# Kernel tuning notes

Measured on AMD Instinct MI355X. Metric: run time of the kernel, lower is better.

Reference implementation:

```python
import jax, jax.numpy as jnp
import numpy as np

N_NODES = 100000
N_EDGES = 1600000
IN_DIM, HIDDEN, OUT_DIM = 128, 64, 32


def setup_inputs() -> dict:
    key = jax.random.key(0)
    k1, k2, k3, k4 = jax.random.split(key, 4)
    x = jax.random.normal(k1, (N_NODES, IN_DIM), dtype=jnp.float32)
    # Glorot-style init for the two GCN linear layers
    W1 = jax.random.normal(k2, (IN_DIM, HIDDEN), dtype=jnp.float32) * (1.0 / np.sqrt(IN_DIM))
    b1 = jnp.zeros((HIDDEN,), dtype=jnp.float32)
    W2 = jax.random.normal(k3, (HIDDEN, OUT_DIM), dtype=jnp.float32) * (1.0 / np.sqrt(HIDDEN))
    b2 = jnp.zeros((OUT_DIM,), dtype=jnp.float32)
    edge_index = jax.random.randint(k4, (2, N_EDGES), 0, N_NODES, dtype=jnp.int32)
    return {"x": x, "W1": W1, "b1": b1, "W2": W2, "b2": b2, "edge_index": edge_index}


def _gcn_norm(edge_index, n_nodes):
    # Add self-loops and compute symmetric normalization D^{-1/2} (A+I) D^{-1/2}
    loops = jnp.arange(n_nodes, dtype=edge_index.dtype)
    src = jnp.concatenate([edge_index[0], loops])  # [E+N]
    dst = jnp.concatenate([edge_index[1], loops])
    deg = jax.ops.segment_sum(jnp.ones_like(dst, dtype=jnp.float32), dst,
                              num_segments=n_nodes)
    dinv = jnp.where(deg > 0, jax.lax.rsqrt(deg), 0.0)
    norm = dinv[src] * dinv[dst]  # [E+N]
    return src, dst, norm


def _gcn_conv(h, W, b, src, dst, norm, n_nodes):
    h = h @ W                                   # [N, out] linear transform first
    msg = h[src] * norm[:, None]                # gather + per-edge scale
    agg = jax.ops.segment_sum(msg, dst, num_segments=n_nodes)  # scatter-add
    return agg + b


def reference(x, W1, b1, W2, b2, edge_index):
    n = x.shape[0]
    src, dst, norm = _gcn_norm(edge_index, n)
    h = jax.nn.relu(_gcn_conv(x, W1, b1, src, dst, norm, n))
    # dropout is identity in eval mode (deterministic reference)
    z = _gcn_conv(h, W2, b2, src, dst, norm, n)
    return z
```

## Files before the change

kernel.cpp:

```cpp
#include <hip/hip_runtime.h>
#include <hip/hip_fp16.h>

#define NB_MAX 784
#define CAP    2560
#define CHUNK  8192

typedef _Float16 half8 __attribute__((ext_vector_type(8)));
typedef float f32x4_t __attribute__((ext_vector_type(4)));
typedef int   i32x4   __attribute__((ext_vector_type(4)));

__device__ inline int   ntld (const int*   p) { return __builtin_nontemporal_load(p); }
__device__ inline i32x4 ntld4(const int*   p) { return __builtin_nontemporal_load((const i32x4*)p); }

__global__ __launch_bounds__(256) void k_bin_gemm1(
        const int* __restrict__ src, const int* __restrict__ dst,
        int* __restrict__ gcur, int* __restrict__ binned, int nb, int e,
        const float* __restrict__ x, const float* __restrict__ W1,
        __half* __restrict__ hp, int n, int binb) {
    __shared__ __align__(16) char smem[64 * 136 * 2];
    const int t = threadIdx.x;

    if (blockIdx.x < binb) {
        int* hist = (int*)smem;
        int* curs = hist + NB_MAX;
        const int base = blockIdx.x * CHUNK;
        const int lim = min(CHUNK, e - base);

        for (int i = t; i < NB_MAX; i += 256) hist[i] = 0;
        __syncthreads();

        const int i4lim = lim >> 2;
        for (int i = t; i < i4lim; i += 256) {
            int4 d = ((const int4*)(dst + base))[i];
            atomicAdd(&hist[d.x >> 7], 1);
            atomicAdd(&hist[d.y >> 7], 1);
            atomicAdd(&hist[d.z >> 7], 1);
            atomicAdd(&hist[d.w >> 7], 1);
        }
        for (int i = (i4lim << 2) + t; i < lim; i += 256)
            atomicAdd(&hist[dst[base + i] >> 7], 1);
        __syncthreads();

        for (int b = t; b < nb; b += 256) {
            int h = hist[b];
            curs[b] = h ? atomicAdd(&gcur[b], h) : 0;
        }
        __syncthreads();

        for (int i = t; i < i4lim; i += 256) {
            i32x4 d = ntld4(dst + base + i * 4);
            i32x4 s = ntld4(src + base + i * 4);
            int o0 = atomicAdd(&curs[d.x >> 7], 1);
            int o1 = atomicAdd(&curs[d.y >> 7], 1);
            int o2 = atomicAdd(&curs[d.z >> 7], 1);
            int o3 = atomicAdd(&curs[d.w >> 7], 1);
            if (o0 < CAP) binned[(size_t)(d.x >> 7) * CAP + o0] = (s.x << 7) | (d.x & 127);
            if (o1 < CAP) binned[(size_t)(d.y >> 7) * CAP + o1] = (s.y << 7) | (d.y & 127);
            if (o2 < CAP) binned[(size_t)(d.z >> 7) * CAP + o2] = (s.z << 7) | (d.z & 127);
            if (o3 < CAP) binned[(size_t)(d.w >> 7) * CAP + o3] = (s.w << 7) | (d.w & 127);
        }
        for (int i = (i4lim << 2) + t; i < lim; i += 256) {
            int d = dst[base + i], s = src[base + i];
            int off = atomicAdd(&curs[d >> 7], 1);
            if (off < CAP) binned[(size_t)(d >> 7) * CAP + off] = (s << 7) | (d & 127);
        }
        return;
    }

    _Float16* wt = (_Float16*)smem;

    for (int i = t; i < 128 * 64; i += 256) {
        int k = i >> 6, o = i & 63;
        wt[o * 136 + k] = (_Float16)W1[i];
    }
    __syncthreads();

    const int lane = t & 63;
    const int wid  = t >> 6;
    const int row0 = (blockIdx.x - binb) * 64 + wid * 16;
    const int rA   = lane & 15;
    const int g    = lane >> 4;

    f32x4_t acc0 = {0.f, 0.f, 0.f, 0.f};
    f32x4_t acc1 = {0.f, 0.f, 0.f, 0.f};
    f32x4_t acc2 = {0.f, 0.f, 0.f, 0.f};
    f32x4_t acc3 = {0.f, 0.f, 0.f, 0.f};

    const int arow = min(row0 + rA, n - 1);
    const float* ap0 = x + (size_t)arow * 128 + g * 8;

#pragma unroll
    for (int ks = 0; ks < 4; ++ks) {
        const float* ap = ap0 + ks * 32;
        float4 a0 = *(const float4*)ap;
        float4 a1 = *(const float4*)(ap + 4);
        half8 af;
        af[0] = (_Float16)a0.x; af[1] = (_Float16)a0.y;
        af[2] = (_Float16)a0.z; af[3] = (_Float16)a0.w;
        af[4] = (_Float16)a1.x; af[5] = (_Float16)a1.y;
        af[6] = (_Float16)a1.z; af[7] = (_Float16)a1.w;

        const _Float16* wb = wt + rA * 136 + ks * 32 + g * 8;
        half8 b0 = *(const half8*)(wb);
        half8 b1 = *(const half8*)(wb + 16 * 136);
        half8 b2 = *(const half8*)(wb + 32 * 136);
        half8 b3 = *(const half8*)(wb + 48 * 136);
        acc0 = __builtin_amdgcn_mfma_f32_16x16x32_f16(af, b0, acc0, 0, 0, 0);
        acc1 = __builtin_amdgcn_mfma_f32_16x16x32_f16(af, b1, acc1, 0, 0, 0);
        acc2 = __builtin_amdgcn_mfma_f32_16x16x32_f16(af, b2, acc2, 0, 0, 0);
        acc3 = __builtin_amdgcn_mfma_f32_16x16x32_f16(af, b3, acc3, 0, 0, 0);
    }

    _Float16* hph = (_Float16*)hp;
#pragma unroll
    for (int r = 0; r < 4; ++r) {
        int node = row0 + g * 4 + r;
        if (node >= n) continue;
        _Float16* o = hph + (size_t)node * 64 + rA;
        o[0]  = (_Float16)acc0[r];
        o[16] = (_Float16)acc1[r];
        o[32] = (_Float16)acc2[r];
        o[48] = (_Float16)acc3[r];
    }
}

__global__ __launch_bounds__(256) void k_sort(const int* __restrict__ binned,
                                              const int* __restrict__ gcur,
                                              int* __restrict__ csr,
                                              int* __restrict__ rpx,
                                              float* __restrict__ dinv,
                                              int n, int e) {
    __shared__ int hist[128], offs[128];
    __shared__ int red[256];
    const int t = threadIdx.x;
    const int b = blockIdx.x;

    int partial = 0;
    for (int j = t; j < b; j += 256) partial += gcur[j];
    red[t] = partial;
    if (t < 128) hist[t] = 0;
    __syncthreads();
    for (int o = 128; o > 0; o >>= 1) {
        if (t < o) red[t] += red[t + o];
        __syncthreads();
    }
    const int base = red[0];
    if (b == 0 && t == 0) rpx[n] = e;

    int sz = gcur[b];
    if (sz > CAP) sz = CAP;
    const int* bp = binned + (size_t)b * CAP;

    const int i4 = sz >> 2;
    for (int i = t; i < i4; i += 256) {
        i32x4 p = ntld4(bp + i * 4);
        atomicAdd(&hist[p.x & 127], 1);
        atomicAdd(&hist[p.y & 127], 1);
        atomicAdd(&hist[p.z & 127], 1);
        atomicAdd(&hist[p.w & 127], 1);
    }
    for (int i = (i4 << 2) + t; i < sz; i += 256)
        atomicAdd(&hist[ntld(bp + i) & 127], 1);
    __syncthreads();

    if (t < 128) offs[t] = hist[t];
    __syncthreads();
    for (int o = 1; o < 128; o <<= 1) {
        int add = (t < 128 && t >= o) ? offs[t - o] : 0;
        __syncthreads();
        if (t < 128) offs[t] += add;
        __syncthreads();
    }

    if (t < 128) {
        int node = (b << 7) + t;
        if (node < n) {
            rpx[node]  = base + offs[t] - hist[t];
            dinv[node] = rsqrtf(1.0f + (float)hist[t]);
        }
    }
    __syncthreads();
    if (t < 128) hist[t] = offs[t] - hist[t];
    __syncthreads();

    for (int i = t; i < sz; i += 256) {
        int p = ntld(bp + i);
        int pos = base + atomicAdd(&hist[p & 127], 1);
        csr[pos] = p >> 7;
    }
}


union Pk8 { float4 f4; __half2 h2[4]; };

__device__ inline void addrow(float acc[8], float4 v) {
    Pk8 u; u.f4 = v;
#pragma unroll
    for (int j = 0; j < 4; ++j) {
        float2 t = __half22float2(u.h2[j]);
        acc[2 * j]     += t.x;
        acc[2 * j + 1] += t.y;
    }
}

__device__ inline void addrow_s(float acc[8], float4 v, float s) {
    Pk8 u; u.f4 = v;
#pragma unroll
    for (int j = 0; j < 4; ++j) {
        float2 t = __half22float2(u.h2[j]);
        acc[2 * j]     = fmaf(t.x, s, acc[2 * j]);
        acc[2 * j + 1] = fmaf(t.y, s, acc[2 * j + 1]);
    }
}

__global__ __launch_bounds__(256) void k_agg1(const int* __restrict__ rpx,
                                              const int* __restrict__ csr,
                                              const __half* __restrict__ hp,
                                              const float* __restrict__ dinv,
                                              const float* __restrict__ b1,
                                              const float* __restrict__ W2,
                                              __half* __restrict__ hp2, int n) {
    __shared__ float w2t[32 * 68];
    __shared__ float tl[32 * 68];
    const int t = threadIdx.x;

    for (int i = t; i < 64 * 32; i += 256) {
        int f = i >> 5, j = i & 31;
        w2t[j * 68 + f] = W2[i];
    }

    const int nl   = t >> 3;
    const int q    = t & 7;
    const int node = blockIdx.x * 32 + nl;
    const bool alive = node < n;

    float acc[8];
#pragma unroll
    for (int j = 0; j < 8; ++j) acc[j] = 0.f;

    float di = 0.f;
    if (alive) {
        const float4* hp4 = (const float4*)hp;
        int start = rpx[node], end = rpx[node + 1];
        di = dinv[node];
        addrow_s(acc, hp4[(size_t)node * 8 + q], di);

        int p = start;
        for (; p + 8 <= end; p += 8) {
            int s[8];
#pragma unroll
            for (int j = 0; j < 8; ++j) s[j] = ntld(csr + p + j);
            float ds[8];
#pragma unroll
            for (int j = 0; j < 8; ++j) ds[j] = dinv[s[j]];
            float4 v[8];
#pragma unroll
            for (int j = 0; j < 8; ++j) v[j] = hp4[(size_t)s[j] * 8 + q];
#pragma unroll
            for (int j = 0; j < 8; ++j) addrow_s(acc, v[j], ds[j]);
        }
        for (; p + 2 <= end; p += 2) {
            int s0 = ntld(csr + p), s1 = ntld(csr + p + 1);
            float d0 = dinv[s0], d1 = dinv[s1];
            float4 v0 = hp4[(size_t)s0 * 8 + q];
            float4 v1 = hp4[(size_t)s1 * 8 + q];
            addrow_s(acc, v0, d0);
            addrow_s(acc, v1, d1);
        }
        if (p < end) {
            int s0 = ntld(csr + p);
            addrow_s(acc, hp4[(size_t)s0 * 8 + q], dinv[s0]);
        }
    }

    float4 ba = ((const float4*)b1)[q * 2];
    float4 bb = ((const float4*)b1)[q * 2 + 1];
    float4 t0, t1;
    t0.x = fmaxf(fmaf(acc[0], di, ba.x), 0.f);
    t0.y = fmaxf(fmaf(acc[1], di, ba.y), 0.f);
    t0.z = fmaxf(fmaf(acc[2], di, ba.z), 0.f);
    t0.w = fmaxf(fmaf(acc[3], di, ba.w), 0.f);
    t1.x = fmaxf(fmaf(acc[4], di, bb.x), 0.f);
    t1.y = fmaxf(fmaf(acc[5], di, bb.y), 0.f);
    t1.z = fmaxf(fmaf(acc[6], di, bb.z), 0.f);
    t1.w = fmaxf(fmaf(acc[7], di, bb.w), 0.f);
    *(float4*)(tl + nl * 68 + q * 8)     = t0;
    *(float4*)(tl + nl * 68 + q * 8 + 4) = t1;
    __syncthreads();

    if (!alive) return;

    const float* trow = tl + nl * 68;
    const float* wa = w2t + q * 68;
    const float* wb = w2t + (q + 8) * 68;
    const float* wc = w2t + (q + 16) * 68;
    const float* wd = w2t + (q + 24) * 68;
    float o0 = 0.f, o1 = 0.f, o2 = 0.f, o3 = 0.f;
#pragma unroll
    for (int f4 = 0; f4 < 16; ++f4) {
        float4 tv = *(const float4*)(trow + f4 * 4);
        float4 v0 = *(const float4*)(wa + f4 * 4);
        float4 v1 = *(const float4*)(wb + f4 * 4);
        float4 v2 = *(const float4*)(wc + f4 * 4);
        float4 v3 = *(const float4*)(wd + f4 * 4);
        o0 += tv.x * v0.x + tv.y * v0.y + tv.z * v0.z + tv.w * v0.w;
        o1 += tv.x * v1.x + tv.y * v1.y + tv.z * v1.z + tv.w * v1.w;
        o2 += tv.x * v2.x + tv.y * v2.y + tv.z * v2.z + tv.w * v2.w;
        o3 += tv.x * v3.x + tv.y * v3.y + tv.z * v3.z + tv.w * v3.w;
    }
    _Float16* hq = (_Float16*)hp2 + (size_t)node * 32;
    hq[q]      = (_Float16)(o0 * di);
    hq[q + 8]  = (_Float16)(o1 * di);
    hq[q + 16] = (_Float16)(o2 * di);
    hq[q + 24] = (_Float16)(o3 * di);
}

template<int LOGF>
__global__ __launch_bounds__(256) void k_aggregate(const int* __restrict__ rpx,
                                                   const int* __restrict__ csr,
                                                   const __half* __restrict__ hp,
                                                   const float* __restrict__ dinv,
                                                   const float* __restrict__ bias,
                                                   float* __restrict__ out, int n) {
    constexpr int F   = 1 << LOGF;
    constexpr int TPN = F / 8;
    int gid  = blockIdx.x * 256 + threadIdx.x;
    int node = gid / TPN;
    int q    = gid % TPN;
    if (node >= n) return;

    const float4* hp4 = (const float4*)hp;
    int start = rpx[node], end = rpx[node + 1];

    float acc[8];
#pragma unroll
    for (int j = 0; j < 8; ++j) acc[j] = 0.f;
    addrow(acc, hp4[(size_t)node * TPN + q]);

    int p = start;
    for (; p + 8 <= end; p += 8) {
        int s[8];
#pragma unroll
        for (int j = 0; j < 8; ++j) s[j] = ntld(csr + p + j);
        float4 v[8];
#pragma unroll
        for (int j = 0; j < 8; ++j) v[j] = hp4[(size_t)s[j] * TPN + q];
#pragma unroll
        for (int j = 0; j < 8; ++j) addrow(acc, v[j]);
    }
    for (; p + 2 <= end; p += 2) {
        int s0 = ntld(csr + p), s1 = ntld(csr + p + 1);
        float4 v0 = hp4[(size_t)s0 * TPN + q];
        float4 v1 = hp4[(size_t)s1 * TPN + q];
        addrow(acc, v0);
        addrow(acc, v1);
    }
    if (p < end)
        addrow(acc, hp4[(size_t)ntld(csr + p) * TPN + q]);

    float di = dinv[node];
    float4 b0 = ((const float4*)bias)[q * 2];
    float4 b1v = ((const float4*)bias)[q * 2 + 1];
    f32x4_t r0, r1;
    r0.x = fmaf(acc[0], di, b0.x); r0.y = fmaf(acc[1], di, b0.y);
    r0.z = fmaf(acc[2], di, b0.z); r0.w = fmaf(acc[3], di, b0.w);
    r1.x = fmaf(acc[4], di, b1v.x); r1.y = fmaf(acc[5], di, b1v.y);
    r1.z = fmaf(acc[6], di, b1v.z); r1.w = fmaf(acc[7], di, b1v.w);
    f32x4_t* o4 = (f32x4_t*)out;
    __builtin_nontemporal_store(r0, o4 + (size_t)node * (F / 4) + q * 2);
    __builtin_nontemporal_store(r1, o4 + (size_t)node * (F / 4) + q * 2 + 1);
}


extern "C" void kernel_launch(void* const* d_in, const int* in_sizes, int n_in,
                              void* d_out, int out_size, void* d_ws, size_t ws_size,
                              hipStream_t stream) {
    const float* x  = (const float*)d_in[0];
    const float* W1 = (const float*)d_in[1];
    const float* b1 = (const float*)d_in[2];
    const float* W2 = (const float*)d_in[3];
    const float* b2 = (const float*)d_in[4];
    const int*   ei = (const int*)d_in[5];

    const int N = in_sizes[0] / 128;
    const int E = in_sizes[5] / 2;
    const int* src = ei;
    const int* dst = ei + E;
    const int NB = (N + 127) >> 7;

    char* w = (char*)d_ws;
    int*    gcur   = (int*)w;                  w += NB_MAX * 4;
    int*    rpx    = (int*)w;                  w += (size_t)(N + 4) * 4;
    float*  dinv   = (float*)w;                w += (size_t)N * 4;
    int*    binned = (int*)w;                  w += (size_t)NB_MAX * CAP * 4;
    int*    csr    = (int*)w;                  w += (size_t)E * 4;
    __half* hp     = (__half*)w;               w += (size_t)N * 64 * 2;
    __half* hp2    = (__half*)w;               w += (size_t)N * 32 * 2;
    float*  out    = (float*)d_out;

    const int binb = (E + CHUNK - 1) / CHUNK;
    const int gb1  = (N + 63) / 64;

    (void)hipMemsetAsync(gcur, 0, NB_MAX * 4, stream);

    k_bin_gemm1<<<binb + gb1, 256, 0, stream>>>(src, dst, gcur, binned, NB, E,
                                                x, W1, hp, N, binb);

    k_sort<<<NB, 256, 0, stream>>>(binned, gcur, csr, rpx, dinv, N, E);

    k_agg1<<<(N + 31) / 32, 256, 0, stream>>>(rpx, csr, hp, dinv, b1, W2, hp2, N);

    k_aggregate<5><<<(N * 4 + 255) / 256, 256, 0, stream>>>(rpx, csr, hp2, dinv, b2, out, N);
}
```

Measured before the change: 146.3 us.

## Split layer-1 neighbor gather into four source-range passes; drop nontemporal hints

The layer-1 aggregation now walks each node's edge list four times, and each pass only gathers sources inside one quarter of the node range. The intent is to keep the working set of gathered fp16 rows small enough to stay in cache. The nontemporal load and store builtins are also replaced with plain loads and stores throughout. The cost is reading the CSR indices four times and adding branch divergence in the inner loop, which can outweigh any cache-locality gain since blocks across the GPU do not run their passes in lockstep.

New measurement: 170.0 us. +16.2%, slower.

```diff
diff --git a/kernel.cpp b/kernel.cpp
--- a/kernel.cpp
+++ b/kernel.cpp
@@ -7,10 +7,6 @@
 
 typedef _Float16 half8 __attribute__((ext_vector_type(8)));
 typedef float f32x4_t __attribute__((ext_vector_type(4)));
-typedef int   i32x4   __attribute__((ext_vector_type(4)));
-
-__device__ inline int   ntld (const int*   p) { return __builtin_nontemporal_load(p); }
-__device__ inline i32x4 ntld4(const int*   p) { return __builtin_nontemporal_load((const i32x4*)p); }
 
 __global__ __launch_bounds__(256) void k_bin_gemm1(
         const int* __restrict__ src, const int* __restrict__ dst,
@@ -48,8 +44,8 @@
         __syncthreads();
 
         for (int i = t; i < i4lim; i += 256) {
-            i32x4 d = ntld4(dst + base + i * 4);
-            i32x4 s = ntld4(src + base + i * 4);
+            int4 d = ((const int4*)(dst + base))[i];
+            int4 s = ((const int4*)(src + base))[i];
             int o0 = atomicAdd(&curs[d.x >> 7], 1);
             int o1 = atomicAdd(&curs[d.y >> 7], 1);
             int o2 = atomicAdd(&curs[d.z >> 7], 1);
@@ -153,14 +149,14 @@
 
     const int i4 = sz >> 2;
     for (int i = t; i < i4; i += 256) {
-        i32x4 p = ntld4(bp + i * 4);
+        int4 p = ((const int4*)bp)[i];
         atomicAdd(&hist[p.x & 127], 1);
         atomicAdd(&hist[p.y & 127], 1);
         atomicAdd(&hist[p.z & 127], 1);
         atomicAdd(&hist[p.w & 127], 1);
     }
     for (int i = (i4 << 2) + t; i < sz; i += 256)
-        atomicAdd(&hist[ntld(bp + i) & 127], 1);
+        atomicAdd(&hist[bp[i] & 127], 1);
     __syncthreads();
 
     if (t < 128) offs[t] = hist[t];
@@ -184,7 +180,7 @@
     __syncthreads();
 
     for (int i = t; i < sz; i += 256) {
-        int p = ntld(bp + i);
+        int p = bp[i];
         int pos = base + atomicAdd(&hist[p & 127], 1);
         csr[pos] = p >> 7;
     }
@@ -241,35 +237,32 @@
     float di = 0.f;
     if (alive) {
         const float4* hp4 = (const float4*)hp;
-        int start = rpx[node], end = rpx[node + 1];
+        const int start = rpx[node], end = rpx[node + 1];
         di = dinv[node];
         addrow_s(acc, hp4[(size_t)node * 8 + q], di);
 
-        int p = start;
-        for (; p + 8 <= end; p += 8) {
-            int s[8];
-#pragma unroll
-            for (int j = 0; j < 8; ++j) s[j] = ntld(csr + p + j);
-            float ds[8];
-#pragma unroll
-            for (int j = 0; j < 8; ++j) ds[j] = dinv[s[j]];
-            float4 v[8];
-#pragma unroll
-            for (int j = 0; j < 8; ++j) v[j] = hp4[(size_t)s[j] * 8 + q];
-#pragma unroll
-            for (int j = 0; j < 8; ++j) addrow_s(acc, v[j], ds[j]);
-        }
-        for (; p + 2 <= end; p += 2) {
-            int s0 = ntld(csr + p), s1 = ntld(csr + p + 1);
-            float d0 = dinv[s0], d1 = dinv[s1];
-            float4 v0 = hp4[(size_t)s0 * 8 + q];
-            float4 v1 = hp4[(size_t)s1 * 8 + q];
-            addrow_s(acc, v0, d0);
-            addrow_s(acc, v1, d1);
-        }
-        if (p < end) {
-            int s0 = ntld(csr + p);
-            addrow_s(acc, hp4[(size_t)s0 * 8 + q], dinv[s0]);
+#pragma unroll 1
+        for (int pass = 0; pass < 4; ++pass) {
+            const int lo = (int)(((long long)n * pass) >> 2);
+            const int hi = (pass == 3) ? n : (int)(((long long)n * (pass + 1)) >> 2);
+            int p = start;
+            for (; p + 8 <= end; p += 8) {
+                int s[8];
+#pragma unroll
+                for (int j = 0; j < 8; ++j) s[j] = csr[p + j];
+#pragma unroll
+                for (int j = 0; j < 8; ++j) {
+                    if (s[j] >= lo && s[j] < hi) {
+                        float ds = dinv[s[j]];
+                        addrow_s(acc, hp4[(size_t)s[j] * 8 + q], ds);
+                    }
+                }
+            }
+            for (; p < end; ++p) {
+                int s0 = csr[p];
+                if (s0 >= lo && s0 < hi)
+                    addrow_s(acc, hp4[(size_t)s0 * 8 + q], dinv[s0]);
+            }
         }
     }
 
@@ -341,7 +334,7 @@
     for (; p + 8 <= end; p += 8) {
         int s[8];
 #pragma unroll
-        for (int j = 0; j < 8; ++j) s[j] = ntld(csr + p + j);
+        for (int j = 0; j < 8; ++j) s[j] = csr[p + j];
         float4 v[8];
 #pragma unroll
         for (int j = 0; j < 8; ++j) v[j] = hp4[(size_t)s[j] * TPN + q];
@@ -349,26 +342,26 @@
         for (int j = 0; j < 8; ++j) addrow(acc, v[j]);
     }
     for (; p + 2 <= end; p += 2) {
-        int s0 = ntld(csr + p), s1 = ntld(csr + p + 1);
+        int s0 = csr[p], s1 = csr[p + 1];
         float4 v0 = hp4[(size_t)s0 * TPN + q];
         float4 v1 = hp4[(size_t)s1 * TPN + q];
         addrow(acc, v0);
         addrow(acc, v1);
     }
     if (p < end)
-        addrow(acc, hp4[(size_t)ntld(csr + p) * TPN + q]);
+        addrow(acc, hp4[(size_t)csr[p] * TPN + q]);
 
     float di = dinv[node];
     float4 b0 = ((const float4*)bias)[q * 2];
     float4 b1v = ((const float4*)bias)[q * 2 + 1];
-    f32x4_t r0, r1;
+    float4 r0, r1;
     r0.x = fmaf(acc[0], di, b0.x); r0.y = fmaf(acc[1], di, b0.y);
     r0.z = fmaf(acc[2], di, b0.z); r0.w = fmaf(acc[3], di, b0.w);
     r1.x = fmaf(acc[4], di, b1v.x); r1.y = fmaf(acc[5], di, b1v.y);
     r1.z = fmaf(acc[6], di, b1v.z); r1.w = fmaf(acc[7], di, b1v.w);
-    f32x4_t* o4 = (f32x4_t*)out;
-    __builtin_nontemporal_store(r0, o4 + (size_t)node * (F / 4) + q * 2);
-    __builtin_nontemporal_store(r1, o4 + (size_t)node * (F / 4) + q * 2 + 1);
+    float4* o4 = (float4*)out;
+    o4[(size_t)node * (F / 4) + q * 2]     = r0;
+    o4[(size_t)node * (F / 4) + q * 2 + 1] = r1;
 }
 
 
```
